# Kernel optimization log

Hardware: AMD Instinct MI355X
Metric: run time of the kernel (lower is better)

## Reference

```python
import jax, jax.numpy as jnp
import numpy as np

N, D, E = 50000, 128, 600000


def setup_inputs() -> dict:
    key = jax.random.key(0)
    k1, k2, k3, k4 = jax.random.split(key, 4)
    x = jax.random.normal(k1, (N, D), dtype=jnp.float32)
    edge_index = jax.random.randint(k2, (2, E), 0, N, dtype=jnp.int64)
    a1 = jax.random.normal(k3, (D, 1), dtype=jnp.float32)
    a2 = jax.random.normal(k4, (D, 1), dtype=jnp.float32)
    bias = jnp.zeros((D,), dtype=jnp.float32)
    return {"x": x, "edge_index": edge_index, "a1": a1, "a2": a2, "bias": bias}


def reference(x, edge_index, a1, a2, bias):
    n = x.shape[0]
    # rank-1 linear: x @ (a1 a2^T) + bias
    x_lin = (x @ a1) * a2.T + bias  # [N, D]

    # add self loops (edge_weight is None path)
    loops = jnp.arange(n, dtype=edge_index.dtype)
    ei = jnp.concatenate([edge_index, jnp.stack([loops, loops])], axis=1)
    row, col = ei[0], ei[1]

    # degree of col (all edge weights are 1)
    ones = jnp.ones(ei.shape[1], dtype=x.dtype)
    deg = jax.ops.segment_sum(ones, col, num_segments=n)  # [N]
    deg_inv_sqrt = jnp.where(deg > 0, jax.lax.rsqrt(deg), 0.0)

    norm = deg_inv_sqrt[row] * deg_inv_sqrt[col]  # [E+N]
    # gather-scale-scatter aggregation
    msgs = norm[:, None] * x_lin[col]  # [E+N, D]
    out = jax.ops.segment_sum(msgs, row, num_segments=n)  # [N, D]
    return out
```

## Files before the change

### kernel.cpp

```cpp
#include <hip/hip_runtime.h>

#define DIM 128
#define CA 64
#define RA 2
#define NA 25000
#define HIST_BLOCKS (CA * RA)
#define CB 32
#define RB 8
#define NB 6250

__global__ __launch_bounds__(1024) void k1_hist_s(
        const float* __restrict__ x, const float* __restrict__ a1,
        const int* __restrict__ col, ushort* __restrict__ pA,
        float* __restrict__ s, int E, int N) {
    __shared__ unsigned h[NA / 2];
    if (blockIdx.x < HIST_BLOCKS) {
        int c  = blockIdx.x % CA;
        int rg = blockIdx.x / CA;
        int lo = rg * NA;
        for (int j = threadIdx.x; j < NA / 2; j += 1024) h[j] = 0u;
        __syncthreads();
        int per = (E + CA - 1) / CA;
        int e0 = c * per;
        int e1 = e0 + per; if (e1 > E) e1 = E;
        for (int e = e0 + threadIdx.x; e < e1; e += 1024) {
            unsigned idx = (unsigned)(col[e] - lo);
            if (idx < (unsigned)NA)
                atomicAdd(&h[idx >> 1], 1u << ((idx & 1) * 16));
        }
        __syncthreads();
        unsigned* dst = (unsigned*)(pA + (size_t)c * N + lo);
        for (int j = threadIdx.x; j < NA / 2; j += 1024) dst[j] = h[j];
    } else {
        int lw   = threadIdx.x >> 6;
        int lane = threadIdx.x & 63;
        int j    = lane & 31;
        int r = ((int)blockIdx.x - HIST_BLOCKS) * 32 + lw * 2 + (lane >> 5);
        if (r >= N) return;
        float4 xv = ((const float4*)x)[(size_t)r * 32 + j];
        float4 av = ((const float4*)a1)[j];
        float p = xv.x * av.x + xv.y * av.y + xv.z * av.z + xv.w * av.w;
        #pragma unroll
        for (int off = 16; off > 0; off >>= 1)
            p += __shfl_xor(p, off, 64);
        if (j == 0) s[r] = p;
    }
}

__global__ void k_combine(const ushort* __restrict__ pA, const float* __restrict__ s,
                          float2* __restrict__ sd, int N) {
    int i = blockIdx.x * blockDim.x + threadIdx.x;
    if (i >= N) return;
    unsigned d = 1u;
    #pragma unroll 8
    for (int c = 0; c < CA; ++c) d += pA[(size_t)c * N + i];
    float dv = rsqrtf((float)d);
    sd[i] = make_float2(dv, dv * s[i]);
}

__global__ __launch_bounds__(1024) void k_histB(const int* __restrict__ row,
                                                const int* __restrict__ col,
                                                const float2* __restrict__ sd,
                                                float2* __restrict__ pB,
                                                int E, int N) {
    __shared__ float up[NB];
    __shared__ float vp[NB];
    int c  = blockIdx.x % CB;
    int rg = blockIdx.x / CB;
    int lo = rg * NB;
    for (int j = threadIdx.x; j < NB; j += 1024) { up[j] = 0.f; vp[j] = 0.f; }
    __syncthreads();
    int per = (E + CB - 1) / CB;
    int e0 = c * per;
    int e1 = e0 + per; if (e1 > E) e1 = E;
    for (int e = e0 + threadIdx.x; e < e1; e += 1024) {
        unsigned idx = (unsigned)(row[e] - lo);
        if (idx < (unsigned)NB) {
            float2 v = sd[col[e]];
            atomicAdd(&up[idx], v.x);
            atomicAdd(&vp[idx], v.y);
        }
    }
    __syncthreads();
    float2* dst = pB + (size_t)c * N + lo;
    for (int j = threadIdx.x; j < NB; j += 1024)
        dst[j] = make_float2(up[j], vp[j]);
}

__global__ __launch_bounds__(256) void k_out(
        const float2* __restrict__ pB, const float2* __restrict__ sd,
        const float* __restrict__ a2, const float* __restrict__ bias,
        float* __restrict__ out, int N) {
    __shared__ float sT[256];
    __shared__ float sW[256];
    int base = blockIdx.x * 256;
    int i = base + threadIdx.x;
    if (i < N) {
        float su = 0.f, sv = 0.f;
        #pragma unroll 8
        for (int c = 0; c < CB; ++c) {
            float2 p = pB[(size_t)c * N + i];
            su += p.x; sv += p.y;
        }
        float2 d = sd[i];
        sT[threadIdx.x] = d.x * (sv + d.y);
        sW[threadIdx.x] = d.x * (su + d.x);
    }
    __syncthreads();
    int j   = threadIdx.x & 31;
    int grp = threadIdx.x >> 5;
    float4 a2v = ((const float4*)a2)[j];
    float4 bv  = ((const float4*)bias)[j];
    #pragma unroll 4
    for (int rep = 0; rep < 32; ++rep) {
        int rl = rep * 8 + grp;
        int node = base + rl;
        if (node >= N) break;
        float T = sT[rl], W = sW[rl];
        float4 o;
        o.x = a2v.x * T + bv.x * W;
        o.y = a2v.y * T + bv.y * W;
        o.z = a2v.z * T + bv.z * W;
        o.w = a2v.w * T + bv.w * W;
        ((float4*)out)[(size_t)node * 32 + j] = o;
    }
}

extern "C" void kernel_launch(void* const* d_in, const int* in_sizes, int n_in,
                              void* d_out, int out_size, void* d_ws, size_t ws_size,
                              hipStream_t stream) {
    const float* x    = (const float*)d_in[0];
    const int*   ei   = (const int*)d_in[1];
    const float* a1   = (const float*)d_in[2];
    const float* a2   = (const float*)d_in[3];
    const float* bias = (const float*)d_in[4];
    float* out = (float*)d_out;

    int N = in_sizes[0] / DIM;
    int E = in_sizes[1] / 2;
    const int* row = ei;
    const int* col = ei + E;

    float*  s  = (float*)d_ws;
    float2* sd = (float2*)(s + N);
    ushort* pA = (ushort*)(sd + N);
    float2* pB = (float2*)(pA + (size_t)CA * N);

    int s_blocks = (N + 31) / 32;
    k1_hist_s<<<HIST_BLOCKS + s_blocks, 1024, 0, stream>>>(x, a1, col, pA, s, E, N);
    k_combine<<<(N + 255) / 256, 256, 0, stream>>>(pA, s, sd, N);
    k_histB  <<<CB * RB, 1024, 0, stream>>>(row, col, sd, pB, E, N);
    k_out    <<<(N + 255) / 256, 256, 0, stream>>>(pB, sd, a2, bias, out, N);
}
```

Measured before the change: 42.69 us.

## Fuse four GCN stages into one cooperative kernel with grid syncs

Replaces four separate kernel launches with a single cooperative persistent kernel of 256 blocks of 1024 threads. The stages are the degree histogram with the x·a1 dot, the degree combine, the row histogram and the output write, separated by grid.sync(). The aim is to remove launch gaps and inter-kernel drain. The combine step now reads packed ushort pairs as 32-bit words. The change risks lower parallelism in the dot and output phases, which now run on fixed grid-stride loops, plus grid-sync overhead, and it falls back to the old multi-kernel path if the cooperative launch fails.

```diff
diff --git a/kernel.cpp b/kernel.cpp
--- a/kernel.cpp
+++ b/kernel.cpp
@@ -1,28 +1,159 @@
 #include <hip/hip_runtime.h>
-
-#define DIM 128
-#define CA 64
-#define RA 2
-#define NA 25000
-#define HIST_BLOCKS (CA * RA)
-#define CB 32
-#define RB 8
-#define NB 6250
+#include <hip/hip_cooperative_groups.h>
+
+namespace cg = cooperative_groups;
+
+#define DIM  128
+#define NBLK 256
+#define NTHR 1024
+#define CA   64
+#define RA   2
+#define NA   25000
+#define HA   (CA * RA)
+#define CB   32
+#define RB   8
+#define NB   6250
+
+struct SM {
+    union {
+        unsigned ha[NA / 2];
+        struct { float up[NB]; float vp[NB]; } hb;
+        struct { float T[256]; float W[256]; } d;
+    };
+};
+
+__global__ __launch_bounds__(NTHR, 4) void mega(
+        const float* __restrict__ x, const int* __restrict__ ei,
+        const float* __restrict__ a1, const float* __restrict__ a2,
+        const float* __restrict__ bias, float* __restrict__ out,
+        ushort* __restrict__ pA, float2* __restrict__ pB,
+        float* __restrict__ s, float2* __restrict__ sd,
+        int N, int E) {
+    __shared__ SM sm;
+    cg::grid_group grid = cg::this_grid();
+    const int* row = ei;
+    const int* col = ei + E;
+    int bid = blockIdx.x, tid = threadIdx.x;
+
+    if (bid < HA) {
+        int c = bid % CA, rg = bid / CA;
+        int lo = rg * NA;
+        for (int j = tid; j < NA / 2; j += NTHR) sm.ha[j] = 0u;
+        __syncthreads();
+        int per = (E + CA - 1) / CA;
+        int e0 = c * per, e1 = e0 + per; if (e1 > E) e1 = E;
+        for (int e = e0 + tid; e < e1; e += NTHR) {
+            unsigned idx = (unsigned)(col[e] - lo);
+            if (idx < (unsigned)NA)
+                atomicAdd(&sm.ha[idx >> 1], 1u << ((idx & 1) * 16));
+        }
+        __syncthreads();
+        unsigned* dst = (unsigned*)(pA + (size_t)c * N + lo);
+        for (int j = tid; j < NA / 2; j += NTHR) dst[j] = sm.ha[j];
+    } else {
+        int sb   = bid - HA;
+        int lane = tid & 63;
+        int j    = lane & 31;
+        int wv   = tid >> 6;
+        float4 av = ((const float4*)a1)[j];
+        int stride = (NBLK - HA) * 32;
+        for (int r = sb * 32 + wv * 2 + (lane >> 5); r < N; r += stride) {
+            float4 xv = ((const float4*)x)[(size_t)r * 32 + j];
+            float p = xv.x * av.x + xv.y * av.y + xv.z * av.z + xv.w * av.w;
+            #pragma unroll
+            for (int off = 16; off > 0; off >>= 1)
+                p += __shfl_xor(p, off, 64);
+            if (j == 0) s[r] = p;
+        }
+    }
+    grid.sync();
+
+    for (int i2 = bid * NTHR + tid; i2 < N / 2; i2 += NBLK * NTHR) {
+        unsigned d0 = 1u, d1 = 1u;
+        #pragma unroll 8
+        for (int c = 0; c < CA; ++c) {
+            unsigned w = *(const unsigned*)&pA[(size_t)c * N + 2 * i2];
+            d0 += w & 0xffffu; d1 += w >> 16;
+        }
+        float dv0 = rsqrtf((float)d0), dv1 = rsqrtf((float)d1);
+        sd[2 * i2]     = make_float2(dv0, dv0 * s[2 * i2]);
+        sd[2 * i2 + 1] = make_float2(dv1, dv1 * s[2 * i2 + 1]);
+    }
+    grid.sync();
+
+    {
+        int c = bid % CB, rg = bid / CB;
+        int lo = rg * NB;
+        for (int j = tid; j < NB; j += NTHR) { sm.hb.up[j] = 0.f; sm.hb.vp[j] = 0.f; }
+        __syncthreads();
+        int per = (E + CB - 1) / CB;
+        int e0 = c * per, e1 = e0 + per; if (e1 > E) e1 = E;
+        for (int e = e0 + tid; e < e1; e += NTHR) {
+            unsigned idx = (unsigned)(row[e] - lo);
+            if (idx < (unsigned)NB) {
+                float2 v = sd[col[e]];
+                atomicAdd(&sm.hb.up[idx], v.x);
+                atomicAdd(&sm.hb.vp[idx], v.y);
+            }
+        }
+        __syncthreads();
+        int len = N - lo; if (len > NB) len = NB;
+        float2* dst = pB + (size_t)c * N + lo;
+        for (int j = tid; j < len; j += NTHR)
+            dst[j] = make_float2(sm.hb.up[j], sm.hb.vp[j]);
+    }
+    grid.sync();
+
+    {
+        int tile = (N + NBLK - 1) / NBLK;
+        int lo = bid * tile;
+        int len = N - lo; if (len > tile) len = tile;
+        if (len > 0) {
+            for (int r = tid; r < len; r += NTHR) {
+                int i = lo + r;
+                float su = 0.f, sv = 0.f;
+                #pragma unroll 8
+                for (int c = 0; c < CB; ++c) {
+                    float2 p = pB[(size_t)c * N + i];
+                    su += p.x; sv += p.y;
+                }
+                float2 dd = sd[i];
+                sm.d.T[r] = dd.x * (sv + dd.y);
+                sm.d.W[r] = dd.x * (su + dd.x);
+            }
+            __syncthreads();
+            int j   = tid & 31;
+            int grp = tid >> 5;
+            float4 a2v = ((const float4*)a2)[j];
+            float4 bv  = ((const float4*)bias)[j];
+            for (int r = grp; r < len; r += 32) {
+                float T = sm.d.T[r], W = sm.d.W[r];
+                float4 o;
+                o.x = a2v.x * T + bv.x * W;
+                o.y = a2v.y * T + bv.y * W;
+                o.z = a2v.z * T + bv.z * W;
+                o.w = a2v.w * T + bv.w * W;
+                ((float4*)out)[(size_t)(lo + r) * 32 + j] = o;
+            }
+        }
+    }
+}
+
+#define FHB 128
 
 __global__ __launch_bounds__(1024) void k1_hist_s(
         const float* __restrict__ x, const float* __restrict__ a1,
         const int* __restrict__ col, ushort* __restrict__ pA,
         float* __restrict__ s, int E, int N) {
     __shared__ unsigned h[NA / 2];
-    if (blockIdx.x < HIST_BLOCKS) {
+    if (blockIdx.x < FHB) {
         int c  = blockIdx.x % CA;
         int rg = blockIdx.x / CA;
         int lo = rg * NA;
         for (int j = threadIdx.x; j < NA / 2; j += 1024) h[j] = 0u;
         __syncthreads();
         int per = (E + CA - 1) / CA;
-        int e0 = c * per;
-        int e1 = e0 + per; if (e1 > E) e1 = E;
+        int e0 = c * per, e1 = e0 + per; if (e1 > E) e1 = E;
         for (int e = e0 + threadIdx.x; e < e1; e += 1024) {
             unsigned idx = (unsigned)(col[e] - lo);
             if (idx < (unsigned)NA)
@@ -35,7 +166,7 @@
         int lw   = threadIdx.x >> 6;
         int lane = threadIdx.x & 63;
         int j    = lane & 31;
-        int r = ((int)blockIdx.x - HIST_BLOCKS) * 32 + lw * 2 + (lane >> 5);
+        int r = ((int)blockIdx.x - FHB) * 32 + lw * 2 + (lane >> 5);
         if (r >= N) return;
         float4 xv = ((const float4*)x)[(size_t)r * 32 + j];
         float4 av = ((const float4*)a1)[j];
@@ -49,13 +180,17 @@
 
 __global__ void k_combine(const ushort* __restrict__ pA, const float* __restrict__ s,
                           float2* __restrict__ sd, int N) {
-    int i = blockIdx.x * blockDim.x + threadIdx.x;
-    if (i >= N) return;
-    unsigned d = 1u;
+    int i2 = blockIdx.x * blockDim.x + threadIdx.x;
+    if (i2 >= N / 2) return;
+    unsigned d0 = 1u, d1 = 1u;
     #pragma unroll 8
-    for (int c = 0; c < CA; ++c) d += pA[(size_t)c * N + i];
-    float dv = rsqrtf((float)d);
-    sd[i] = make_float2(dv, dv * s[i]);
+    for (int c = 0; c < CA; ++c) {
+        unsigned w = *(const unsigned*)&pA[(size_t)c * N + 2 * i2];
+        d0 += w & 0xffffu; d1 += w >> 16;
+    }
+    float dv0 = rsqrtf((float)d0), dv1 = rsqrtf((float)d1);
+    sd[2 * i2]     = make_float2(dv0, dv0 * s[2 * i2]);
+    sd[2 * i2 + 1] = make_float2(dv1, dv1 * s[2 * i2 + 1]);
 }
 
 __global__ __launch_bounds__(1024) void k_histB(const int* __restrict__ row,
@@ -71,8 +206,7 @@
     for (int j = threadIdx.x; j < NB; j += 1024) { up[j] = 0.f; vp[j] = 0.f; }
     __syncthreads();
     int per = (E + CB - 1) / CB;
-    int e0 = c * per;
-    int e1 = e0 + per; if (e1 > E) e1 = E;
+    int e0 = c * per, e1 = e0 + per; if (e1 > E) e1 = E;
     for (int e = e0 + threadIdx.x; e < e1; e += 1024) {
         unsigned idx = (unsigned)(row[e] - lo);
         if (idx < (unsigned)NB) {
@@ -82,8 +216,9 @@
         }
     }
     __syncthreads();
+    int len = N - lo; if (len > NB) len = NB;
     float2* dst = pB + (size_t)c * N + lo;
-    for (int j = threadIdx.x; j < NB; j += 1024)
+    for (int j = threadIdx.x; j < len; j += 1024)
         dst[j] = make_float2(up[j], vp[j]);
 }
 
@@ -146,9 +281,16 @@
     ushort* pA = (ushort*)(sd + N);
     float2* pB = (float2*)(pA + (size_t)CA * N);
 
-    int s_blocks = (N + 31) / 32;
-    k1_hist_s<<<HIST_BLOCKS + s_blocks, 1024, 0, stream>>>(x, a1, col, pA, s, E, N);
-    k_combine<<<(N + 255) / 256, 256, 0, stream>>>(pA, s, sd, N);
-    k_histB  <<<CB * RB, 1024, 0, stream>>>(row, col, sd, pB, E, N);
-    k_out    <<<(N + 255) / 256, 256, 0, stream>>>(pB, sd, a2, bias, out, N);
-}
+    void* args[] = { (void*)&x, (void*)&ei, (void*)&a1, (void*)&a2, (void*)&bias,
+                     (void*)&out, (void*)&pA, (void*)&pB, (void*)&s, (void*)&sd,
+                     (void*)&N, (void*)&E };
+    hipError_t rc = hipLaunchCooperativeKernel((const void*)mega, dim3(NBLK),
+                                               dim3(NTHR), args, 0, stream);
+    if (rc != hipSuccess) {
+        int s_blocks = (N + 31) / 32;
+        k1_hist_s<<<FHB + s_blocks, 1024, 0, stream>>>(x, a1, col, pA, s, E, N);
+        k_combine<<<(N / 2 + 255) / 256, 256, 0, stream>>>(pA, s, sd, N);
+        k_histB  <<<CB * RB, 1024, 0, stream>>>(row, col, sd, pB, E, N);
+        k_out    <<<(N + 255) / 256, 256, 0, stream>>>(pB, sd, a2, bias, out, N);
+    }
+}
```

New measurement: 157.7 us. 269% more time.
